# Optimization experiments

Measured on AMD Instinct MI355X. Metric: run time of the kernel, lower is better.

The kernel has to match this reference:

```python
import jax, jax.numpy as jnp
import numpy as np
from jax import lax

HEADS = 8
PS = 4  # window size


def setup_inputs() -> dict:
    key = jax.random.key(0)
    k1, k2, k3, k4 = jax.random.split(key, 4)
    b, c, h, w = 8, 256, 128, 128
    x = jax.random.normal(k1, (b, c, h, w), dtype=jnp.float32)
    W_qkv = jax.random.normal(k2, (3 * c, c), dtype=jnp.float32) * 0.05
    W_dw = jax.random.normal(k3, (3 * c, 1, 3, 3), dtype=jnp.float32) * 0.1
    temperature = jnp.ones((HEADS, 1, 1), dtype=jnp.float32)
    W_proj = jax.random.normal(k4, (c, c), dtype=jnp.float32) * 0.05
    return {"x": x, "W_qkv": W_qkv, "W_dw": W_dw, "temperature": temperature, "W_proj": W_proj}


def _l2norm(t, eps=1e-12):
    # matches torch F.normalize(dim=-1): x / max(||x||_2, eps)
    n = jnp.sqrt(jnp.sum(t * t, axis=-1, keepdims=True))
    return t / jnp.maximum(n, eps)


def reference(x, W_qkv, W_dw, temperature, W_proj):
    b, c, h0, w0 = x.shape
    ps, heads = PS, HEADS
    pad_h = (ps - h0 % ps) % ps
    pad_w = (ps - w0 % ps) % ps
    if pad_h or pad_w:
        x = jnp.pad(x, ((0, 0), (0, 0), (0, pad_h), (0, pad_w)))
    H, W = x.shape[2], x.shape[3]
    nh, nw = H // ps, W // ps
    d = c // heads

    # 1x1 conv -> depthwise 3x3 conv (groups = 3c, padding 1)
    qkv = jnp.einsum('oc,bchw->bohw', W_qkv, x)
    qkv = lax.conv_general_dilated(qkv, W_dw, (1, 1), 'SAME',
                                   feature_group_count=3 * c,
                                   dimension_numbers=('NCHW', 'OIHW', 'NCHW'))
    q, k, v = jnp.split(qkv, 3, axis=1)

    def win(t):
        # b (head d) (nh ps) (nw ps) -> b (nh nw) head d (ps ps)
        t = t.reshape(b, heads, d, nh, ps, nw, ps)
        t = t.transpose(0, 3, 5, 1, 2, 4, 6)  # b nh nw head d ps ps
        return t.reshape(b, nh * nw, heads, d, ps * ps)

    q, k, v = win(q), win(k), win(v)
    q = _l2norm(q)
    k = _l2norm(k)

    # channel attention over head-dim d, keys/queries live in the ps*ps window
    attn = jnp.einsum('bnhde,bnhfe->bnhdf', q, k) * temperature  # (b,n,head,d,d)
    attn = jax.nn.softmax(attn, axis=-1)
    out = jnp.einsum('bnhdf,bnhfe->bnhde', attn, v)  # (b,n,head,d,ps*ps)

    # inverse rearrange -> b (head d) H W
    out = out.reshape(b, nh, nw, heads, d, ps, ps)
    out = out.transpose(0, 3, 4, 1, 5, 2, 6).reshape(b, c, H, W)
    out = jnp.einsum('oc,bchw->bohw', W_proj, out)
    if pad_h or pad_w:
        out = out[:, :, :h0, :w0]
    return out
```

## Files before the change

### kernel.cpp

```cpp
#include <hip/hip_runtime.h>
#include <math.h>


#define HW_ (128*128)
#define CHW_ (256*128*128)

typedef __attribute__((ext_vector_type(8))) short short8;
typedef __attribute__((ext_vector_type(4))) float f32x4;

static __device__ __forceinline__ unsigned short f2bf(float f) {
    unsigned int u = __float_as_uint(f);
    unsigned int r = (u + 0x7fffu + ((u >> 16) & 1u)) >> 16;
    return (unsigned short)r;
}
static __device__ __forceinline__ float bf2f(unsigned short u) {
    return __uint_as_float(((unsigned int)u) << 16);
}

__global__ __launch_bounds__(256) void conv_w(
    const float* __restrict__ Wq, const float* __restrict__ Wp,
    unsigned short* __restrict__ out)
{
    int i = blockIdx.x * 256 + threadIdx.x;
    float v = (i < 196608) ? Wq[i] : Wp[i - 196608];
    out[i] = f2bf(v);
}

__global__ __launch_bounds__(256) void conv_xt(
    const float* __restrict__ xs, unsigned short* __restrict__ xT)
{
    __shared__ float tile[64][65];
    const int t = threadIdx.x;
    const int p0 = blockIdx.x * 64, c0 = blockIdx.y * 64;
    const float* xb = xs + (size_t)blockIdx.z * CHW_;
    unsigned short* xTb = xT + (size_t)blockIdx.z * HW_ * 256;
    {
        const int cl = t >> 4, pl = (t & 15) * 4;
        #pragma unroll
        for (int i = 0; i < 4; ++i) {
            float4 v = *reinterpret_cast<const float4*>(
                xb + (size_t)(c0 + cl + i * 16) * HW_ + p0 + pl);
            tile[cl + i * 16][pl + 0] = v.x;
            tile[cl + i * 16][pl + 1] = v.y;
            tile[cl + i * 16][pl + 2] = v.z;
            tile[cl + i * 16][pl + 3] = v.w;
        }
    }
    __syncthreads();
    #pragma unroll
    for (int i = 0; i < 2; ++i) {
        int chunk = i * 256 + t;
        int pr = chunk >> 3, c8 = (chunk & 7) * 8;
        short8 o;
        #pragma unroll
        for (int j = 0; j < 8; ++j)
            o[j] = (short)f2bf(tile[c8 + j][pr]);
        *reinterpret_cast<short8*>(xTb + (size_t)(p0 + pr) * 256 + c0 + c8) = o;
    }
}

template<int BF16OUT>
__global__ __launch_bounds__(256) void gemm_bf16(
    const unsigned short* __restrict__ A,
    const unsigned short* __restrict__ Bt,
    void* __restrict__ Cv,
    size_t strideBatch)
{
    __shared__ __align__(16) char smem[BF16OUT ? 16896 : 16384];
    unsigned short* Asm = (unsigned short*)smem;
    unsigned short* Bsm = (unsigned short*)(smem + 8192);

    const int t = threadIdx.x;
    const int lane = t & 63, wid = t >> 6;
    const int m0 = blockIdx.y * 128, n0 = blockIdx.x * 128;
    const int nb = n0 >> 14, nloc0 = n0 & 16383;
    const int wr = wid >> 1, wc = wid & 1;
    const int l15 = lane & 15, l4 = lane >> 4;

    const unsigned short* srcA[2];
    const unsigned short* srcB[2];
    #pragma unroll
    for (int i = 0; i < 2; ++i) {
        int u = i * 256 + t;
        int r = u >> 2, cs = u & 3;
        int c = cs ^ ((r ^ (r >> 2)) & 3);
        srcA[i] = A  + (size_t)(m0 + r) * 256 + c * 8;
        srcB[i] = Bt + (size_t)(n0 + r) * 256 + c * 8;
    }

    int ar[4], br[4];
    #pragma unroll
    for (int i = 0; i < 4; ++i) {
        int rm = wr * 64 + i * 16 + l15;
        ar[i] = rm * 4 + (l4 ^ ((rm ^ (rm >> 2)) & 3));
        int rn = wc * 64 + i * 16 + l15;
        br[i] = rn * 4 + (l4 ^ ((rn ^ (rn >> 2)) & 3));
    }

    f32x4 acc[4][4];
    #pragma unroll
    for (int i = 0; i < 4; ++i)
        #pragma unroll
        for (int j = 0; j < 4; ++j)
            acc[i][j] = (f32x4){0.f, 0.f, 0.f, 0.f};

    const short8* Ab = (const short8*)Asm;
    const short8* Bb = (const short8*)Bsm;

    for (int k0 = 0; k0 < 256; k0 += 32) {
        __syncthreads();
        #pragma unroll
        for (int i = 0; i < 2; ++i) {
            __builtin_amdgcn_global_load_lds(
                (const __attribute__((address_space(1))) void*)(srcA[i] + k0),
                (__attribute__((address_space(3))) void*)(smem + i * 4096 + wid * 1024),
                16, 0, 0);
            __builtin_amdgcn_global_load_lds(
                (const __attribute__((address_space(1))) void*)(srcB[i] + k0),
                (__attribute__((address_space(3))) void*)(smem + 8192 + i * 4096 + wid * 1024),
                16, 0, 0);
        }
        __syncthreads();
        short8 af[4], bf[4];
        #pragma unroll
        for (int i = 0; i < 4; ++i) { af[i] = Ab[ar[i]]; bf[i] = Bb[br[i]]; }
        #pragma unroll
        for (int am = 0; am < 4; ++am)
            #pragma unroll
            for (int bn = 0; bn < 4; ++bn)
                acc[am][bn] = __builtin_amdgcn_mfma_f32_16x16x32_bf16(
                    af[am], bf[bn], acc[am][bn], 0, 0, 0);
    }

    if (BF16OUT) {
        unsigned short* Co = (unsigned short*)Cv + (size_t)nb * strideBatch + nloc0;
        float* ep = (float*)smem;
        const int rr = t >> 3, c0 = (t & 7) * 16;
        #pragma unroll
        for (int am = 0; am < 4; ++am) {
            __syncthreads();
            #pragma unroll
            for (int q = 0; q < 4; ++q)
                #pragma unroll
                for (int bn = 0; bn < 4; ++bn)
                    ep[(wr * 16 + l4 * 4 + q) * 132 + wc * 64 + bn * 16 + l15] =
                        acc[am][bn][q];
            __syncthreads();
            short8 o0, o1;
            #pragma unroll
            for (int j = 0; j < 8; ++j) {
                o0[j] = (short)f2bf(ep[rr * 132 + c0 + j]);
                o1[j] = (short)f2bf(ep[rr * 132 + c0 + 8 + j]);
            }
            int m = m0 + (rr >> 4) * 64 + am * 16 + (rr & 15);
            unsigned short* p = Co + (size_t)m * 16384 + c0;
            *reinterpret_cast<short8*>(p) = o0;
            *reinterpret_cast<short8*>(p + 8) = o1;
        }
    } else {
        float* Co = (float*)Cv + (size_t)nb * strideBatch + nloc0;
        #pragma unroll
        for (int am = 0; am < 4; ++am)
            #pragma unroll
            for (int q = 0; q < 4; ++q) {
                int m = m0 + wr * 64 + am * 16 + l4 * 4 + q;
                #pragma unroll
                for (int bn = 0; bn < 4; ++bn)
                    Co[(size_t)m * 16384 + wc * 64 + bn * 16 + l15] =
                        acc[am][bn][q];
            }
    }
}

__global__ __launch_bounds__(256) void dwconv_win(
    const unsigned short* __restrict__ qkv,
    const float* __restrict__ Wdw,
    unsigned short* __restrict__ dww)
{
    const int t    = threadIdx.x;
    const int lane = t & 63;
    const int iw   = t & 31;
    const int chl  = t >> 5;
    const int wyl  = blockIdx.x;
    const int ch   = blockIdx.y * 8 + chl;
    const int bz   = blockIdx.z;

    float w[9];
    #pragma unroll
    for (int i = 0; i < 9; ++i) w[i] = Wdw[ch * 9 + i];

    float h[6][6];
    const unsigned short* plane = qkv + (size_t)(bz * 768 + ch) * HW_;
    #pragma unroll
    for (int r = 0; r < 6; ++r) {
        int gy = wyl * 4 - 1 + r;
        float c0 = 0.f, c1 = 0.f, c2 = 0.f, c3 = 0.f;
        if (gy >= 0 && gy < 128) {
            ushort4 u = *reinterpret_cast<const ushort4*>(
                plane + (size_t)gy * 128 + iw * 4);
            c0 = bf2f(u.x); c1 = bf2f(u.y); c2 = bf2f(u.z); c3 = bf2f(u.w);
        }
        float lf = __shfl(c3, (lane + 63) & 63);
        float rt = __shfl(c0, (lane + 1) & 63);
        h[r][0] = (iw == 0)  ? 0.f : lf;
        h[r][1] = c0; h[r][2] = c1; h[r][3] = c2; h[r][4] = c3;
        h[r][5] = (iw == 31) ? 0.f : rt;
    }

    unsigned short* outp =
        dww + ((size_t)(bz * 1024 + wyl * 32 + iw) * 768 + ch) * 16;
    short8 o0, o1;
    #pragma unroll
    for (int py = 0; py < 4; ++py) {
        #pragma unroll
        for (int px = 0; px < 4; ++px) {
            float s = 0.f;
            #pragma unroll
            for (int dy = 0; dy < 3; ++dy)
                #pragma unroll
                for (int dx = 0; dx < 3; ++dx)
                    s += h[py + dy][px + dx] * w[dy * 3 + dx];
            int e = py * 4 + px;
            if (e < 8) o0[e] = (short)f2bf(s); else o1[e - 8] = (short)f2bf(s);
        }
    }
    *reinterpret_cast<short8*>(outp) = o0;
    *reinterpret_cast<short8*>(outp + 8) = o1;
}

__global__ __launch_bounds__(256) void attn2(
    const unsigned short* __restrict__ dww,
    const float* __restrict__ temp,
    unsigned short* __restrict__ attnT)
{
    __shared__ float kv[512 * 20];
    const int t   = threadIdx.x;
    const int iw  = blockIdx.x;
    const int wyl = blockIdx.y;
    const int bz  = blockIdx.z;
    const int win = bz * 1024 + wyl * 32 + iw;
    const unsigned short* src = dww + (size_t)win * 12288;

    float q[16], kr[16], vr[16];
    {
        short8 a0 = *reinterpret_cast<const short8*>(src + t * 16);
        short8 a1 = *reinterpret_cast<const short8*>(src + t * 16 + 8);
        short8 b0 = *reinterpret_cast<const short8*>(src + (256 + t) * 16);
        short8 b1 = *reinterpret_cast<const short8*>(src + (256 + t) * 16 + 8);
        short8 c0 = *reinterpret_cast<const short8*>(src + (512 + t) * 16);
        short8 c1 = *reinterpret_cast<const short8*>(src + (512 + t) * 16 + 8);
        #pragma unroll
        for (int j = 0; j < 8; ++j) {
            q[j]      = bf2f((unsigned short)a0[j]);
            q[8 + j]  = bf2f((unsigned short)a1[j]);
            kr[j]     = bf2f((unsigned short)b0[j]);
            kr[8 + j] = bf2f((unsigned short)b1[j]);
            vr[j]     = bf2f((unsigned short)c0[j]);
            vr[8 + j] = bf2f((unsigned short)c1[j]);
        }
    }

    {
        float sq = 0.f, sk = 0.f;
        #pragma unroll
        for (int e = 0; e < 16; ++e) { sq += q[e] * q[e]; sk += kr[e] * kr[e]; }
        float cq = 1.0f / fmaxf(sqrtf(sq), 1e-12f);
        float ck = 1.0f / fmaxf(sqrtf(sk), 1e-12f);
        #pragma unroll
        for (int e = 0; e < 16; ++e) { q[e] *= cq; kr[e] *= ck; }
    }

    {
        float* kp = &kv[t * 20];
        float* vp = &kv[(256 + t) * 20];
        #pragma unroll
        for (int j = 0; j < 4; ++j) {
            *reinterpret_cast<float4*>(kp + j * 4) =
                make_float4(kr[j*4], kr[j*4+1], kr[j*4+2], kr[j*4+3]);
            *reinterpret_cast<float4*>(vp + j * 4) =
                make_float4(vr[j*4], vr[j*4+1], vr[j*4+2], vr[j*4+3]);
        }
    }
    __syncthreads();

    const int head = t >> 5;
    const float tmpv = temp[head];
    const float* kb = &kv[(head * 32) * 20];
    const float* vb = &kv[(256 + head * 32) * 20];

    float lg[32];
    float mx = -1e30f;
    #pragma unroll
    for (int f = 0; f < 32; ++f) {
        float s = 0.f;
        #pragma unroll
        for (int j = 0; j < 4; ++j) {
            float4 k4 = *reinterpret_cast<const float4*>(kb + f * 20 + j * 4);
            s += q[j*4] * k4.x + q[j*4+1] * k4.y + q[j*4+2] * k4.z + q[j*4+3] * k4.w;
        }
        s *= tmpv;
        lg[f] = s;
        mx = fmaxf(mx, s);
    }
    float sum = 0.f;
    #pragma unroll
    for (int f = 0; f < 32; ++f) { lg[f] = __expf(lg[f] - mx); sum += lg[f]; }
    const float inv = 1.0f / sum;

    float o[16];
    #pragma unroll
    for (int e = 0; e < 16; ++e) o[e] = 0.f;
    #pragma unroll
    for (int f = 0; f < 32; ++f) {
        float p = lg[f];
        #pragma unroll
        for (int j = 0; j < 4; ++j) {
            float4 v4 = *reinterpret_cast<const float4*>(vb + f * 20 + j * 4);
            o[j*4]   += p * v4.x; o[j*4+1] += p * v4.y;
            o[j*4+2] += p * v4.z; o[j*4+3] += p * v4.w;
        }
    }

    #pragma unroll
    for (int e = 0; e < 16; ++e) {
        int py = e >> 2, px = e & 3;
        size_t pl = (size_t)bz * HW_ + (wyl * 4 + py) * 128 + iw * 4 + px;
        attnT[pl * 256 + t] = f2bf(o[e] * inv);
    }
}

extern "C" void kernel_launch(void* const* d_in, const int* in_sizes, int n_in,
                              void* d_out, int out_size, void* d_ws, size_t ws_size,
                              hipStream_t stream) {
    const float* x     = (const float*)d_in[0];
    const float* Wqkv  = (const float*)d_in[1];
    const float* Wdw   = (const float*)d_in[2];
    const float* temp  = (const float*)d_in[3];
    const float* Wproj = (const float*)d_in[4];
    float* out = (float*)d_out;

    unsigned short* Wb = (unsigned short*)d_ws;
    const size_t offW = 262144 * 2;

    const size_t xtB  = (size_t)HW_ * 256 * 2;
    const size_t qkvB = (size_t)768 * HW_ * 2;
    const size_t dwwB = (size_t)1024 * 768 * 16 * 2;
    const size_t atB  = (size_t)HW_ * 256 * 2;
    const size_t perB = xtB + qkvB + dwwB + atB;

    int G = 8;
    while (G > 1 && offW + (size_t)G * perB > ws_size) G >>= 1;

    unsigned short* xT    = (unsigned short*)((char*)d_ws + offW);
    unsigned short* qkv   = (unsigned short*)((char*)d_ws + offW + (size_t)G * xtB);
    unsigned short* dww   = (unsigned short*)((char*)d_ws + offW + (size_t)G * (xtB + qkvB));
    unsigned short* attnT = (unsigned short*)((char*)d_ws + offW + (size_t)G * (xtB + qkvB + dwwB));

    conv_w<<<1024, 256, 0, stream>>>(Wqkv, Wproj, Wb);

    for (int b0 = 0; b0 < 8; b0 += G) {
        conv_xt<<<dim3(HW_ / 64, 4, G), 256, 0, stream>>>(
            x + (size_t)b0 * CHW_, xT);

        gemm_bf16<1><<<dim3(G * 128, 6), 256, 0, stream>>>(
            Wb, xT, qkv, (size_t)768 * HW_);

        dwconv_win<<<dim3(32, 96, G), 256, 0, stream>>>(
            qkv, Wdw, dww);

        attn2<<<dim3(32, 32, G), 256, 0, stream>>>(
            dww, temp, attnT);

        gemm_bf16<0><<<dim3(G * 128, 2), 256, 0, stream>>>(
            Wb + 196608, attnT, out + (size_t)b0 * CHW_, (size_t)CHW_);
    }
}
```

Before: 394.2 us.

## Fuse fp32-to-bf16 input transpose into QKV GEMM B-tile loading

Removes the separate conv_xt kernel that transposed x to a bf16 pixel-major buffer. The new gemm_qkv kernel reads fp32 x directly, converts to bf16 in registers and writes a B tile to LDS, with an LDS-staged epilogue writing bf16 qkv. The batch group size drops from 8 to 4. This saves a full write and reread of the transposed activation. In exchange, B loads become scalar strided reads, the 6 M-blocks each reload x, and the LDS read pattern for B fragments changes.

```diff
diff --git a/kernel.cpp b/kernel.cpp
--- a/kernel.cpp
+++ b/kernel.cpp
@@ -6,6 +6,7 @@
 #define CHW_ (256*128*128)
 
 typedef __attribute__((ext_vector_type(8))) short short8;
+typedef __attribute__((ext_vector_type(4))) short shortv4;
 typedef __attribute__((ext_vector_type(4))) float f32x4;
 
 static __device__ __forceinline__ unsigned short f2bf(float f) {
@@ -26,36 +27,118 @@
     out[i] = f2bf(v);
 }
 
-__global__ __launch_bounds__(256) void conv_xt(
-    const float* __restrict__ xs, unsigned short* __restrict__ xT)
+__global__ __launch_bounds__(256) void gemm_qkv(
+    const unsigned short* __restrict__ A,
+    const float* __restrict__ x,
+    unsigned short* __restrict__ qkv)
 {
-    __shared__ float tile[64][65];
+    __shared__ __align__(16) char smem[16896];
+    shortv4* Bq = (shortv4*)(smem + 8192);
+
     const int t = threadIdx.x;
-    const int p0 = blockIdx.x * 64, c0 = blockIdx.y * 64;
-    const float* xb = xs + (size_t)blockIdx.z * CHW_;
-    unsigned short* xTb = xT + (size_t)blockIdx.z * HW_ * 256;
-    {
-        const int cl = t >> 4, pl = (t & 15) * 4;
+    const int lane = t & 63, wid = t >> 6;
+    const int m0 = blockIdx.x * 128;
+    const int by = blockIdx.y;
+    const int nb = by >> 7;
+    const int nloc0 = (by & 127) * 128;
+    const int wr = wid >> 1, wc = wid & 1;
+    const int l15 = lane & 15, l4 = lane >> 4;
+
+    const unsigned short* srcA[2];
+    #pragma unroll
+    for (int i = 0; i < 2; ++i) {
+        int u = i * 256 + t;
+        int r = u >> 2, cs = u & 3;
+        int c = cs ^ ((r ^ (r >> 2)) & 3);
+        srcA[i] = A + (size_t)(m0 + r) * 256 + c * 8;
+    }
+    int ar[4];
+    #pragma unroll
+    for (int i = 0; i < 4; ++i) {
+        int rm = wr * 64 + i * 16 + l15;
+        ar[i] = rm * 4 + (l4 ^ ((rm ^ (rm >> 2)) & 3));
+    }
+
+    const int tp = t & 127, th = t >> 7;
+    const float* xb = x + (size_t)nb * CHW_ + nloc0 + tp;
+
+    f32x4 acc[4][4];
+    #pragma unroll
+    for (int i = 0; i < 4; ++i)
+        #pragma unroll
+        for (int j = 0; j < 4; ++j)
+            acc[i][j] = (f32x4){0.f, 0.f, 0.f, 0.f};
+
+    const short8* Ab = (const short8*)smem;
+
+    for (int k0 = 0; k0 < 256; k0 += 32) {
+        __syncthreads();
+        float bv[16];
+        #pragma unroll
+        for (int j = 0; j < 4; ++j)
+            #pragma unroll
+            for (int i = 0; i < 4; ++i)
+                bv[j * 4 + i] = xb[(size_t)(k0 + th * 16 + j * 4 + i) * HW_];
+        #pragma unroll
+        for (int i = 0; i < 2; ++i)
+            __builtin_amdgcn_global_load_lds(
+                (const __attribute__((address_space(1))) void*)(srcA[i] + k0),
+                (__attribute__((address_space(3))) void*)(smem + i * 4096 + wid * 1024),
+                16, 0, 0);
+        #pragma unroll
+        for (int j = 0; j < 4; ++j) {
+            shortv4 s;
+            s.x = (short)f2bf(bv[j * 4 + 0]);
+            s.y = (short)f2bf(bv[j * 4 + 1]);
+            s.z = (short)f2bf(bv[j * 4 + 2]);
+            s.w = (short)f2bf(bv[j * 4 + 3]);
+            Bq[(th * 4 + j) * 128 + tp] = s;
+        }
+        __syncthreads();
+
+        short8 af[4], bf[4];
         #pragma unroll
         for (int i = 0; i < 4; ++i) {
-            float4 v = *reinterpret_cast<const float4*>(
-                xb + (size_t)(c0 + cl + i * 16) * HW_ + p0 + pl);
-            tile[cl + i * 16][pl + 0] = v.x;
-            tile[cl + i * 16][pl + 1] = v.y;
-            tile[cl + i * 16][pl + 2] = v.z;
-            tile[cl + i * 16][pl + 3] = v.w;
-        }
-    }
-    __syncthreads();
-    #pragma unroll
-    for (int i = 0; i < 2; ++i) {
-        int chunk = i * 256 + t;
-        int pr = chunk >> 3, c8 = (chunk & 7) * 8;
-        short8 o;
-        #pragma unroll
-        for (int j = 0; j < 8; ++j)
-            o[j] = (short)f2bf(tile[c8 + j][pr]);
-        *reinterpret_cast<short8*>(xTb + (size_t)(p0 + pr) * 256 + c0 + c8) = o;
+            af[i] = Ab[ar[i]];
+            int rn = wc * 64 + i * 16 + l15;
+            shortv4 lo = Bq[(l4 * 2) * 128 + rn];
+            shortv4 hi = Bq[(l4 * 2 + 1) * 128 + rn];
+            short8 b;
+            b[0] = lo.x; b[1] = lo.y; b[2] = lo.z; b[3] = lo.w;
+            b[4] = hi.x; b[5] = hi.y; b[6] = hi.z; b[7] = hi.w;
+            bf[i] = b;
+        }
+        #pragma unroll
+        for (int am = 0; am < 4; ++am)
+            #pragma unroll
+            for (int bn = 0; bn < 4; ++bn)
+                acc[am][bn] = __builtin_amdgcn_mfma_f32_16x16x32_bf16(
+                    af[am], bf[bn], acc[am][bn], 0, 0, 0);
+    }
+
+    unsigned short* Co = qkv + (size_t)nb * (768 * (size_t)HW_) + nloc0;
+    float* ep = (float*)smem;
+    const int rr = t >> 3, c0 = (t & 7) * 16;
+    #pragma unroll
+    for (int am = 0; am < 4; ++am) {
+        __syncthreads();
+        #pragma unroll
+        for (int q = 0; q < 4; ++q)
+            #pragma unroll
+            for (int bn = 0; bn < 4; ++bn)
+                ep[(wr * 16 + l4 * 4 + q) * 132 + wc * 64 + bn * 16 + l15] =
+                    acc[am][bn][q];
+        __syncthreads();
+        short8 o0, o1;
+        #pragma unroll
+        for (int j = 0; j < 8; ++j) {
+            o0[j] = (short)f2bf(ep[rr * 132 + c0 + j]);
+            o1[j] = (short)f2bf(ep[rr * 132 + c0 + 8 + j]);
+        }
+        int m = m0 + (rr >> 4) * 64 + am * 16 + (rr & 15);
+        unsigned short* p = Co + (size_t)m * 16384 + c0;
+        *reinterpret_cast<short8*>(p) = o0;
+        *reinterpret_cast<short8*>(p + 8) = o1;
     }
 }
 
@@ -67,8 +150,6 @@
     size_t strideBatch)
 {
     __shared__ __align__(16) char smem[BF16OUT ? 16896 : 16384];
-    unsigned short* Asm = (unsigned short*)smem;
-    unsigned short* Bsm = (unsigned short*)(smem + 8192);
 
     const int t = threadIdx.x;
     const int lane = t & 63, wid = t >> 6;
@@ -104,8 +185,8 @@
         for (int j = 0; j < 4; ++j)
             acc[i][j] = (f32x4){0.f, 0.f, 0.f, 0.f};
 
-    const short8* Ab = (const short8*)Asm;
-    const short8* Bb = (const short8*)Bsm;
+    const short8* Ab = (const short8*)smem;
+    const short8* Bb = (const short8*)(smem + 8192);
 
     for (int k0 = 0; k0 < 256; k0 += 32) {
         __syncthreads();
@@ -342,28 +423,23 @@
     unsigned short* Wb = (unsigned short*)d_ws;
     const size_t offW = 262144 * 2;
 
-    const size_t xtB  = (size_t)HW_ * 256 * 2;
     const size_t qkvB = (size_t)768 * HW_ * 2;
     const size_t dwwB = (size_t)1024 * 768 * 16 * 2;
     const size_t atB  = (size_t)HW_ * 256 * 2;
-    const size_t perB = xtB + qkvB + dwwB + atB;
-
-    int G = 8;
+    const size_t perB = qkvB + dwwB + atB;
+
+    int G = 4;
     while (G > 1 && offW + (size_t)G * perB > ws_size) G >>= 1;
 
-    unsigned short* xT    = (unsigned short*)((char*)d_ws + offW);
-    unsigned short* qkv   = (unsigned short*)((char*)d_ws + offW + (size_t)G * xtB);
-    unsigned short* dww   = (unsigned short*)((char*)d_ws + offW + (size_t)G * (xtB + qkvB));
-    unsigned short* attnT = (unsigned short*)((char*)d_ws + offW + (size_t)G * (xtB + qkvB + dwwB));
+    unsigned short* qkv   = (unsigned short*)((char*)d_ws + offW);
+    unsigned short* dww   = (unsigned short*)((char*)d_ws + offW + (size_t)G * qkvB);
+    unsigned short* attnT = (unsigned short*)((char*)d_ws + offW + (size_t)G * (qkvB + dwwB));
 
     conv_w<<<1024, 256, 0, stream>>>(Wqkv, Wproj, Wb);
 
     for (int b0 = 0; b0 < 8; b0 += G) {
-        conv_xt<<<dim3(HW_ / 64, 4, G), 256, 0, stream>>>(
-            x + (size_t)b0 * CHW_, xT);
-
-        gemm_bf16<1><<<dim3(G * 128, 6), 256, 0, stream>>>(
-            Wb, xT, qkv, (size_t)768 * HW_);
+        gemm_qkv<<<dim3(6, G * 128), 256, 0, stream>>>(
+            Wb, x + (size_t)b0 * CHW_, qkv);
 
         dwconv_win<<<dim3(32, 96, G), 256, 0, stream>>>(
             qkv, Wdw, dww);
```

Measured after the change: 410.3 us. 1.04x slower.

## Swap GEMM grid axes for tile reuse and store attention K/V as bf16 in LDS

Applied to the files above, without the earlier changes.

The GEMM grid now puts the M tiles on blockIdx.x, so consecutive blocks share the same activation (B) tile and differ only in weight rows. This should improve L2 reuse of the large activation operand. The attention kernel now keeps normalized K and raw V in shared memory as bf16 with a 24-element padded stride instead of fp32, which halves LDS footprint and traffic and allows higher occupancy. In exchange it adds an extra bf16 rounding of the normalized K and more conversion instructions in the inner loops.

```diff
diff --git a/kernel.cpp b/kernel.cpp
--- a/kernel.cpp
+++ b/kernel.cpp
@@ -67,12 +67,11 @@
     size_t strideBatch)
 {
     __shared__ __align__(16) char smem[BF16OUT ? 16896 : 16384];
-    unsigned short* Asm = (unsigned short*)smem;
-    unsigned short* Bsm = (unsigned short*)(smem + 8192);
 
     const int t = threadIdx.x;
     const int lane = t & 63, wid = t >> 6;
-    const int m0 = blockIdx.y * 128, n0 = blockIdx.x * 128;
+    const int m0 = blockIdx.x * 128;
+    const int n0 = blockIdx.y * 128;
     const int nb = n0 >> 14, nloc0 = n0 & 16383;
     const int wr = wid >> 1, wc = wid & 1;
     const int l15 = lane & 15, l4 = lane >> 4;
@@ -104,8 +103,8 @@
         for (int j = 0; j < 4; ++j)
             acc[i][j] = (f32x4){0.f, 0.f, 0.f, 0.f};
 
-    const short8* Ab = (const short8*)Asm;
-    const short8* Bb = (const short8*)Bsm;
+    const short8* Ab = (const short8*)smem;
+    const short8* Bb = (const short8*)(smem + 8192);
 
     for (int k0 = 0; k0 < 256; k0 += 32) {
         __syncthreads();
@@ -233,7 +232,7 @@
     const float* __restrict__ temp,
     unsigned short* __restrict__ attnT)
 {
-    __shared__ float kv[512 * 20];
+    __shared__ unsigned short kv[512 * 24];
     const int t   = threadIdx.x;
     const int iw  = blockIdx.x;
     const int wyl = blockIdx.y;
@@ -241,23 +240,20 @@
     const int win = bz * 1024 + wyl * 32 + iw;
     const unsigned short* src = dww + (size_t)win * 12288;
 
-    float q[16], kr[16], vr[16];
-    {
-        short8 a0 = *reinterpret_cast<const short8*>(src + t * 16);
-        short8 a1 = *reinterpret_cast<const short8*>(src + t * 16 + 8);
-        short8 b0 = *reinterpret_cast<const short8*>(src + (256 + t) * 16);
-        short8 b1 = *reinterpret_cast<const short8*>(src + (256 + t) * 16 + 8);
-        short8 c0 = *reinterpret_cast<const short8*>(src + (512 + t) * 16);
-        short8 c1 = *reinterpret_cast<const short8*>(src + (512 + t) * 16 + 8);
-        #pragma unroll
-        for (int j = 0; j < 8; ++j) {
-            q[j]      = bf2f((unsigned short)a0[j]);
-            q[8 + j]  = bf2f((unsigned short)a1[j]);
-            kr[j]     = bf2f((unsigned short)b0[j]);
-            kr[8 + j] = bf2f((unsigned short)b1[j]);
-            vr[j]     = bf2f((unsigned short)c0[j]);
-            vr[8 + j] = bf2f((unsigned short)c1[j]);
-        }
+    short8 b0 = *reinterpret_cast<const short8*>(src + (256 + t) * 16);
+    short8 b1 = *reinterpret_cast<const short8*>(src + (256 + t) * 16 + 8);
+    short8 c0 = *reinterpret_cast<const short8*>(src + (512 + t) * 16);
+    short8 c1 = *reinterpret_cast<const short8*>(src + (512 + t) * 16 + 8);
+    short8 a0 = *reinterpret_cast<const short8*>(src + t * 16);
+    short8 a1 = *reinterpret_cast<const short8*>(src + t * 16 + 8);
+
+    float q[16], kr[16];
+    #pragma unroll
+    for (int j = 0; j < 8; ++j) {
+        q[j]      = bf2f((unsigned short)a0[j]);
+        q[8 + j]  = bf2f((unsigned short)a1[j]);
+        kr[j]     = bf2f((unsigned short)b0[j]);
+        kr[8 + j] = bf2f((unsigned short)b1[j]);
     }
 
     {
@@ -269,34 +265,35 @@
         #pragma unroll
         for (int e = 0; e < 16; ++e) { q[e] *= cq; kr[e] *= ck; }
     }
-
-    {
-        float* kp = &kv[t * 20];
-        float* vp = &kv[(256 + t) * 20];
-        #pragma unroll
-        for (int j = 0; j < 4; ++j) {
-            *reinterpret_cast<float4*>(kp + j * 4) =
-                make_float4(kr[j*4], kr[j*4+1], kr[j*4+2], kr[j*4+3]);
-            *reinterpret_cast<float4*>(vp + j * 4) =
-                make_float4(vr[j*4], vr[j*4+1], vr[j*4+2], vr[j*4+3]);
-        }
-    }
+    short8 kn0, kn1;
+    #pragma unroll
+    for (int j = 0; j < 8; ++j) {
+        kn0[j] = (short)f2bf(kr[j]);
+        kn1[j] = (short)f2bf(kr[8 + j]);
+    }
+
+    *reinterpret_cast<short8*>(&kv[t * 24])             = kn0;
+    *reinterpret_cast<short8*>(&kv[t * 24 + 8])         = kn1;
+    *reinterpret_cast<short8*>(&kv[(256 + t) * 24])     = c0;
+    *reinterpret_cast<short8*>(&kv[(256 + t) * 24 + 8]) = c1;
     __syncthreads();
 
     const int head = t >> 5;
     const float tmpv = temp[head];
-    const float* kb = &kv[(head * 32) * 20];
-    const float* vb = &kv[(256 + head * 32) * 20];
+    const unsigned short* kb = &kv[(head * 32) * 24];
+    const unsigned short* vb = &kv[(256 + head * 32) * 24];
 
     float lg[32];
     float mx = -1e30f;
     #pragma unroll
     for (int f = 0; f < 32; ++f) {
+        short8 k0 = *reinterpret_cast<const short8*>(kb + f * 24);
+        short8 k1 = *reinterpret_cast<const short8*>(kb + f * 24 + 8);
         float s = 0.f;
         #pragma unroll
-        for (int j = 0; j < 4; ++j) {
-            float4 k4 = *reinterpret_cast<const float4*>(kb + f * 20 + j * 4);
-            s += q[j*4] * k4.x + q[j*4+1] * k4.y + q[j*4+2] * k4.z + q[j*4+3] * k4.w;
+        for (int j = 0; j < 8; ++j) {
+            s += q[j]     * bf2f((unsigned short)k0[j]);
+            s += q[8 + j] * bf2f((unsigned short)k1[j]);
         }
         s *= tmpv;
         lg[f] = s;
@@ -312,12 +309,13 @@
     for (int e = 0; e < 16; ++e) o[e] = 0.f;
     #pragma unroll
     for (int f = 0; f < 32; ++f) {
+        short8 v0 = *reinterpret_cast<const short8*>(vb + f * 24);
+        short8 v1 = *reinterpret_cast<const short8*>(vb + f * 24 + 8);
         float p = lg[f];
         #pragma unroll
-        for (int j = 0; j < 4; ++j) {
-            float4 v4 = *reinterpret_cast<const float4*>(vb + f * 20 + j * 4);
-            o[j*4]   += p * v4.x; o[j*4+1] += p * v4.y;
-            o[j*4+2] += p * v4.z; o[j*4+3] += p * v4.w;
+        for (int j = 0; j < 8; ++j) {
+            o[j]     += p * bf2f((unsigned short)v0[j]);
+            o[8 + j] += p * bf2f((unsigned short)v1[j]);
         }
     }
 
@@ -362,7 +360,7 @@
         conv_xt<<<dim3(HW_ / 64, 4, G), 256, 0, stream>>>(
             x + (size_t)b0 * CHW_, xT);
 
-        gemm_bf16<1><<<dim3(G * 128, 6), 256, 0, stream>>>(
+        gemm_bf16<1><<<dim3(6, G * 128), 256, 0, stream>>>(
             Wb, xT, qkv, (size_t)768 * HW_);
 
         dwconv_win<<<dim3(32, 96, G), 256, 0, stream>>>(
@@ -371,7 +369,7 @@
         attn2<<<dim3(32, 32, G), 256, 0, stream>>>(
             dww, temp, attnT);
 
-        gemm_bf16<0><<<dim3(G * 128, 2), 256, 0, stream>>>(
+        gemm_bf16<0><<<dim3(2, G * 128), 256, 0, stream>>>(
             Wb + 196608, attnT, out + (size_t)b0 * CHW_, (size_t)CHW_);
     }
 }
```

Measured after the change: 413.4 us. +4.9%, slower.
